# Performance work log

Measured on AMD Instinct MI355X. Metric: run time of the kernel, lower is better.

The kernel has to match this reference:

```python
import jax, jax.numpy as jnp
import numpy as np

MARGIN = 1.0
EPS = 1e-12


def setup_inputs() -> dict:
    key = jax.random.key(0)
    k1, k2, k3 = jax.random.split(key, 3)
    B, C, D = 16384, 500, 512
    features = jax.random.normal(k1, (B, D), dtype=jnp.float32)
    prototypes = jax.random.normal(k2, (C, D), dtype=jnp.float32)
    labels = jax.random.randint(k3, (B,), 0, C, dtype=jnp.int64)
    return {"features": features, "prototypes": prototypes, "labels": labels}


def reference(features, prototypes, labels):
    # Pairwise L2 distances [B, C] via the expanded form (no [B,C,D] intermediate)
    f2 = jnp.sum(features * features, axis=-1, keepdims=True)   # [B, 1]
    p2 = jnp.sum(prototypes * prototypes, axis=-1)               # [C]
    sq = f2 + p2 - 2.0 * (features @ prototypes.T)               # [B, C]
    dists = jnp.sqrt(jnp.maximum(sq, EPS))                       # [B, C]

    B, C = dists.shape
    d_pos = jnp.take_along_axis(dists, labels[:, None], axis=1)[:, 0]  # [B]
    pos_mask = jax.nn.one_hot(labels, C, dtype=bool)             # [B, C]
    d_neg_min = jnp.min(jnp.where(pos_mask, jnp.inf, dists), axis=-1)  # [B]

    loss = jnp.mean(jax.nn.relu(d_pos - d_neg_min + MARGIN))
    return loss
```

## Files before the change

kernel.cpp:

```cpp
#include <hip/hip_runtime.h>
#include <stdint.h>
#include <stddef.h>

#define BB 16384
#define CC 500
#define DD 512
#define PADC 512
#define LMARGIN 1.0f
#define EPSQ 1e-12f

#define GROUP_P 32
#define N_GROUPS (PADC / GROUP_P)
#define ROWB 1040

typedef __attribute__((ext_vector_type(8))) _Float16 f16x8;
typedef __attribute__((ext_vector_type(4))) float f32x4;

#define GLOBAL_AS __attribute__((address_space(1)))
#define LDS_AS __attribute__((address_space(3)))

__device__ __forceinline__ void ld_lds16(const void* g, void* l) {
  __builtin_amdgcn_global_load_lds((const GLOBAL_AS void*)g, (LDS_AS void*)l, 16, 0, 0);
}

__device__ __forceinline__ unsigned short f2h_bits(float f) {
  union { _Float16 h; unsigned short u; } v;
  v.h = (_Float16)f;
  return v.u;
}

__global__ void prep_kernel(const float* __restrict__ protos,
                            unsigned short* __restrict__ protoH,
                            float* __restrict__ p2) {
  int c = blockIdx.x;
  int t = threadIdx.x;
  float v0 = 0.f, v1 = 0.f;
  if (c < CC) {
    v0 = protos[c * DD + 2 * t];
    v1 = protos[c * DD + 2 * t + 1];
  }
  unsigned pk = (unsigned)f2h_bits(v0) | ((unsigned)f2h_bits(v1) << 16);
  ((unsigned*)protoH)[c * (DD / 2) + t] = pk;
  float s = v0 * v0 + v1 * v1;
#pragma unroll
  for (int d = 1; d < 64; d <<= 1) s += __shfl_xor(s, d, 64);
  __shared__ float ws4[4];
  if ((t & 63) == 0) ws4[t >> 6] = s;
  __syncthreads();
  if (t == 0) p2[c] = ws4[0] + ws4[1] + ws4[2] + ws4[3];
}

__launch_bounds__(256, 1)
__global__ void loss_kernel(const float* __restrict__ feat,
                            const int* __restrict__ labels,
                            const unsigned short* __restrict__ protoH,
                            const float* __restrict__ p2,
                            float* __restrict__ out) {
  __shared__ __align__(16) unsigned char ldsB[GROUP_P * ROWB];
  __shared__ float f2s[4][16];
  __shared__ float wsum[4];

  const int tid = threadIdx.x;
  const int wave = tid >> 6;
  const int lane = tid & 63;
  const int lane16 = lane & 15;
  const int quad = lane >> 4;
  const int rowBase = blockIdx.x * 64 + wave * 16;

#pragma unroll
  for (int r = 0; r < 8; ++r) {
    int p = wave * 8 + r;
    ld_lds16(protoH + (size_t)p * DD + lane * 8, ldsB + p * ROWB);
  }

  f16x8 afrag[16];
  float f2part = 0.f;
  const float* frow = feat + (size_t)(rowBase + lane16) * DD;
#pragma unroll
  for (int s = 0; s < 16; ++s) {
    const int k0 = s * 32 + quad * 8;
    f32x4 a0 = *(const f32x4*)(frow + k0);
    f32x4 a1 = *(const f32x4*)(frow + k0 + 4);
    f16x8 af;
#pragma unroll
    for (int j = 0; j < 4; ++j) {
      af[j] = (_Float16)a0[j];
      af[j + 4] = (_Float16)a1[j];
      f2part = fmaf(a0[j], a0[j], f2part);
      f2part = fmaf(a1[j], a1[j], f2part);
    }
    afrag[s] = af;
  }
  f2part += __shfl_xor(f2part, 16, 64);
  f2part += __shfl_xor(f2part, 32, 64);
  if (quad == 0) f2s[wave][lane16] = f2part;

  int lab[4];
#pragma unroll
  for (int i = 0; i < 4; ++i) lab[i] = labels[rowBase + quad * 4 + i];

  __syncthreads();

  float f2r[4];
#pragma unroll
  for (int i = 0; i < 4; ++i) f2r[i] = f2s[wave][quad * 4 + i];

  float runMin[4], posD[4];
#pragma unroll
  for (int i = 0; i < 4; ++i) { runMin[i] = 1e30f; posD[i] = -1e30f; }

  for (int g = 0; g < N_GROUPS; ++g) {
    f32x4 acc0 = {0.f, 0.f, 0.f, 0.f};
    f32x4 acc1 = {0.f, 0.f, 0.f, 0.f};
    const unsigned char* bbase = ldsB + lane16 * ROWB + quad * 16;
#pragma unroll
    for (int s = 0; s < 16; ++s) {
      f16x8 b0 = *(const f16x8*)(bbase + s * 64);
      f16x8 b1 = *(const f16x8*)(bbase + 16 * ROWB + s * 64);
      acc0 = __builtin_amdgcn_mfma_f32_16x16x32_f16(afrag[s], b0, acc0, 0, 0, 0);
      acc1 = __builtin_amdgcn_mfma_f32_16x16x32_f16(afrag[s], b1, acc1, 0, 0, 0);
    }
    __syncthreads();
    if (g + 1 < N_GROUPS) {
#pragma unroll
      for (int r = 0; r < 8; ++r) {
        int p = wave * 8 + r;
        ld_lds16(protoH + (size_t)((g + 1) * GROUP_P + p) * DD + lane * 8,
                 ldsB + p * ROWB);
      }
    }
    const int col0 = g * GROUP_P + lane16;
    const int col1 = col0 + 16;
    const float p20 = p2[col0];
    const float p21 = p2[col1];
#pragma unroll
    for (int i = 0; i < 4; ++i) {
      float d0 = sqrtf(fmaxf(f2r[i] + p20 - 2.f * acc0[i], EPSQ));
      float d1 = sqrtf(fmaxf(f2r[i] + p21 - 2.f * acc1[i], EPSQ));
      bool isPos0 = (col0 == lab[i]);
      bool isPos1 = (col1 == lab[i]);
      posD[i] = fmaxf(posD[i], isPos0 ? d0 : -1e30f);
      posD[i] = fmaxf(posD[i], isPos1 ? d1 : -1e30f);
      runMin[i] = fminf(runMin[i], (!isPos0 && col0 < CC) ? d0 : 1e30f);
      runMin[i] = fminf(runMin[i], (!isPos1 && col1 < CC) ? d1 : 1e30f);
    }
    __syncthreads();
  }

  float termSum = 0.f;
#pragma unroll
  for (int i = 0; i < 4; ++i) {
    float m = runMin[i], p = posD[i];
#pragma unroll
    for (int d = 1; d < 16; d <<= 1) {
      m = fminf(m, __shfl_xor(m, d, 64));
      p = fmaxf(p, __shfl_xor(p, d, 64));
    }
    termSum += fmaxf(p - m + LMARGIN, 0.f);
  }
  float contrib = (lane16 == 0) ? termSum : 0.f;
#pragma unroll
  for (int d = 1; d < 64; d <<= 1) contrib += __shfl_xor(contrib, d, 64);
  if (lane == 0) wsum[wave] = contrib;
  __syncthreads();
  if (tid == 0)
    atomicAdd(out, (wsum[0] + wsum[1] + wsum[2] + wsum[3]) * (1.0f / BB));
}

extern "C" void kernel_launch(void* const* d_in, const int* in_sizes, int n_in,
                              void* d_out, int out_size, void* d_ws, size_t ws_size,
                              hipStream_t stream) {
  const float* feat = (const float*)d_in[0];
  const float* protos = (const float*)d_in[1];
  const int* labels = (const int*)d_in[2];
  float* out = (float*)d_out;

  unsigned short* protoH = (unsigned short*)d_ws;
  float* p2 = (float*)((char*)d_ws + (size_t)PADC * DD * sizeof(unsigned short));

  hipMemsetAsync(d_out, 0, sizeof(float) * (out_size > 0 ? out_size : 1), stream);
  prep_kernel<<<PADC, 256, 0, stream>>>(protos, protoH, p2);
  loss_kernel<<<BB / 64, 256, 0, stream>>>(feat, labels, protoH, p2, out);
}
```

Before: 107.9 us.

## Restructure into fp16 prepass plus 2D-tiled MFMA GEMM with partial-reduction kernel

Replaces the single fused loss kernel with four stages. Features are converted to fp16 in a separate pass, a 128x128 tiled GEMM with double-buffered LDS staging writes per-row partial min/positive distances for each column tile, and a final kernel reduces them into the loss. The host memset is dropped and the output is zeroed inside the prototype prep kernel. The aim is better data reuse and more parallelism (a 2D grid, two blocks per CU), at the cost of an extra fp16 feature round trip through memory, more launches, and reliance on the zeroing kernel running before the atomic adds.

```diff
diff --git a/kernel.cpp b/kernel.cpp
--- a/kernel.cpp
+++ b/kernel.cpp
@@ -8,10 +8,7 @@
 #define PADC 512
 #define LMARGIN 1.0f
 #define EPSQ 1e-12f
-
-#define GROUP_P 32
-#define N_GROUPS (PADC / GROUP_P)
-#define ROWB 1040
+#define NK 16
 
 typedef __attribute__((ext_vector_type(8))) _Float16 f16x8;
 typedef __attribute__((ext_vector_type(4))) float f32x4;
@@ -23,148 +20,189 @@
   __builtin_amdgcn_global_load_lds((const GLOBAL_AS void*)g, (LDS_AS void*)l, 16, 0, 0);
 }
 
-__device__ __forceinline__ unsigned short f2h_bits(float f) {
-  union { _Float16 h; unsigned short u; } v;
-  v.h = (_Float16)f;
-  return v.u;
-}
-
-__global__ void prep_kernel(const float* __restrict__ protos,
-                            unsigned short* __restrict__ protoH,
-                            float* __restrict__ p2) {
-  int c = blockIdx.x;
-  int t = threadIdx.x;
-  float v0 = 0.f, v1 = 0.f;
+__global__ void prepP_kernel(const float* __restrict__ protos,
+                             unsigned short* __restrict__ protoH,
+                             float* __restrict__ p2,
+                             float* __restrict__ out) {
+  int c = blockIdx.x * 4 + (threadIdx.x >> 6);
+  int lane = threadIdx.x & 63;
+  if (c == 0 && lane == 0) out[0] = 0.f;
+  f32x4 a0 = {0.f, 0.f, 0.f, 0.f}, a1 = a0;
   if (c < CC) {
-    v0 = protos[c * DD + 2 * t];
-    v1 = protos[c * DD + 2 * t + 1];
-  }
-  unsigned pk = (unsigned)f2h_bits(v0) | ((unsigned)f2h_bits(v1) << 16);
-  ((unsigned*)protoH)[c * (DD / 2) + t] = pk;
-  float s = v0 * v0 + v1 * v1;
+    const float* src = protos + (size_t)c * DD + lane * 8;
+    a0 = *(const f32x4*)src;
+    a1 = *(const f32x4*)(src + 4);
+  }
+  f16x8 h;
+  float s = 0.f;
+#pragma unroll
+  for (int u = 0; u < 4; ++u) {
+    h[u] = (_Float16)a0[u];
+    h[u + 4] = (_Float16)a1[u];
+    s = fmaf(a0[u], a0[u], s);
+    s = fmaf(a1[u], a1[u], s);
+  }
+  *(f16x8*)(protoH + (size_t)c * DD + lane * 8) = h;
 #pragma unroll
   for (int d = 1; d < 64; d <<= 1) s += __shfl_xor(s, d, 64);
-  __shared__ float ws4[4];
-  if ((t & 63) == 0) ws4[t >> 6] = s;
-  __syncthreads();
-  if (t == 0) p2[c] = ws4[0] + ws4[1] + ws4[2] + ws4[3];
-}
-
-__launch_bounds__(256, 1)
-__global__ void loss_kernel(const float* __restrict__ feat,
+  if (lane == 0) p2[c] = s;
+}
+
+__global__ void prepF_kernel(const float* __restrict__ feat,
+                             unsigned short* __restrict__ featH,
+                             float* __restrict__ f2) {
+  int row = blockIdx.x * 4 + (threadIdx.x >> 6);
+  int lane = threadIdx.x & 63;
+  const float* src = feat + (size_t)row * DD + lane * 8;
+  f32x4 a0 = *(const f32x4*)src;
+  f32x4 a1 = *(const f32x4*)(src + 4);
+  f16x8 h;
+  float s = 0.f;
+#pragma unroll
+  for (int u = 0; u < 4; ++u) {
+    h[u] = (_Float16)a0[u];
+    h[u + 4] = (_Float16)a1[u];
+    s = fmaf(a0[u], a0[u], s);
+    s = fmaf(a1[u], a1[u], s);
+  }
+  *(f16x8*)(featH + (size_t)row * DD + lane * 8) = h;
+#pragma unroll
+  for (int d = 1; d < 64; d <<= 1) s += __shfl_xor(s, d, 64);
+  if (lane == 0) f2[row] = s;
+}
+
+__launch_bounds__(256, 2)
+__global__ void gemm_kernel(const unsigned short* __restrict__ featH,
+                            const unsigned short* __restrict__ protoH,
+                            const float* __restrict__ f2,
+                            const float* __restrict__ p2,
                             const int* __restrict__ labels,
-                            const unsigned short* __restrict__ protoH,
-                            const float* __restrict__ p2,
-                            float* __restrict__ out) {
-  __shared__ __align__(16) unsigned char ldsB[GROUP_P * ROWB];
-  __shared__ float f2s[4][16];
-  __shared__ float wsum[4];
+                            float2* __restrict__ ws2) {
+  __shared__ __align__(16) unsigned short Ab[2][128 * 32];
+  __shared__ __align__(16) unsigned short Bb[2][128 * 32];
+  __shared__ float f2l[128], p2l[128];
+  __shared__ int labl[128];
+  __shared__ float redM[2][128], redP[2][128];
 
   const int tid = threadIdx.x;
-  const int wave = tid >> 6;
+  const int w = tid >> 6;
   const int lane = tid & 63;
   const int lane16 = lane & 15;
   const int quad = lane >> 4;
-  const int rowBase = blockIdx.x * 64 + wave * 16;
-
-#pragma unroll
-  for (int r = 0; r < 8; ++r) {
-    int p = wave * 8 + r;
-    ld_lds16(protoH + (size_t)p * DD + lane * 8, ldsB + p * ROWB);
-  }
-
-  f16x8 afrag[16];
-  float f2part = 0.f;
-  const float* frow = feat + (size_t)(rowBase + lane16) * DD;
-#pragma unroll
-  for (int s = 0; s < 16; ++s) {
-    const int k0 = s * 32 + quad * 8;
-    f32x4 a0 = *(const f32x4*)(frow + k0);
-    f32x4 a1 = *(const f32x4*)(frow + k0 + 4);
-    f16x8 af;
-#pragma unroll
-    for (int j = 0; j < 4; ++j) {
-      af[j] = (_Float16)a0[j];
-      af[j + 4] = (_Float16)a1[j];
-      f2part = fmaf(a0[j], a0[j], f2part);
-      f2part = fmaf(a1[j], a1[j], f2part);
-    }
-    afrag[s] = af;
-  }
-  f2part += __shfl_xor(f2part, 16, 64);
-  f2part += __shfl_xor(f2part, 32, 64);
-  if (quad == 0) f2s[wave][lane16] = f2part;
-
-  int lab[4];
-#pragma unroll
-  for (int i = 0; i < 4; ++i) lab[i] = labels[rowBase + quad * 4 + i];
+  const int wm = w & 1;
+  const int wn = w >> 1;
+  const int r0 = blockIdx.x * 128;
+  const int c0 = blockIdx.y * 128;
+
+  const int srow = w * 16 + (lane >> 2);
+  const int sbyte = (lane & 3) * 16;
+  const char* gA = (const char*)featH + ((size_t)(r0 + srow) * DD) * 2 + sbyte;
+  const char* gB = (const char*)protoH + ((size_t)(c0 + srow) * DD) * 2 + sbyte;
+
+#define STAGE(kc, buf)                                                       \
+  do {                                                                       \
+    char* lA = (char*)&Ab[buf][0] + w * 1024 + lane * 16;                    \
+    char* lB = (char*)&Bb[buf][0] + w * 1024 + lane * 16;                    \
+    ld_lds16(gA + (kc) * 64, lA);                                            \
+    ld_lds16(gA + (kc) * 64 + (size_t)64 * DD * 2, lA + 4096);               \
+    ld_lds16(gB + (kc) * 64, lB);                                            \
+    ld_lds16(gB + (kc) * 64 + (size_t)64 * DD * 2, lB + 4096);               \
+  } while (0)
+
+  STAGE(0, 0);
+
+  if (tid < 128) {
+    f2l[tid] = f2[r0 + tid];
+    p2l[tid] = p2[c0 + tid];
+    labl[tid] = labels[r0 + tid];
+  }
+
+  f32x4 acc[4][4];
+#pragma unroll
+  for (int ms = 0; ms < 4; ++ms)
+#pragma unroll
+    for (int ns = 0; ns < 4; ++ns) acc[ms][ns] = (f32x4){0.f, 0.f, 0.f, 0.f};
 
   __syncthreads();
 
-  float f2r[4];
-#pragma unroll
-  for (int i = 0; i < 4; ++i) f2r[i] = f2s[wave][quad * 4 + i];
-
-  float runMin[4], posD[4];
-#pragma unroll
-  for (int i = 0; i < 4; ++i) { runMin[i] = 1e30f; posD[i] = -1e30f; }
-
-  for (int g = 0; g < N_GROUPS; ++g) {
-    f32x4 acc0 = {0.f, 0.f, 0.f, 0.f};
-    f32x4 acc1 = {0.f, 0.f, 0.f, 0.f};
-    const unsigned char* bbase = ldsB + lane16 * ROWB + quad * 16;
-#pragma unroll
-    for (int s = 0; s < 16; ++s) {
-      f16x8 b0 = *(const f16x8*)(bbase + s * 64);
-      f16x8 b1 = *(const f16x8*)(bbase + 16 * ROWB + s * 64);
-      acc0 = __builtin_amdgcn_mfma_f32_16x16x32_f16(afrag[s], b0, acc0, 0, 0, 0);
-      acc1 = __builtin_amdgcn_mfma_f32_16x16x32_f16(afrag[s], b1, acc1, 0, 0, 0);
-    }
+  int buf = 0;
+  for (int kc = 0; kc < NK; ++kc) {
+    if (kc + 1 < NK) STAGE(kc + 1, buf ^ 1);
+
+    f16x8 af[4], bfr[4];
+#pragma unroll
+    for (int ms = 0; ms < 4; ++ms)
+      af[ms] = *(const f16x8*)(&Ab[buf][(wm * 64 + ms * 16 + lane16) * 32 +
+                                        quad * 8]);
+#pragma unroll
+    for (int ns = 0; ns < 4; ++ns)
+      bfr[ns] = *(const f16x8*)(&Bb[buf][(wn * 64 + ns * 16 + lane16) * 32 +
+                                         quad * 8]);
+#pragma unroll
+    for (int ms = 0; ms < 4; ++ms)
+#pragma unroll
+      for (int ns = 0; ns < 4; ++ns)
+        acc[ms][ns] = __builtin_amdgcn_mfma_f32_16x16x32_f16(
+            af[ms], bfr[ns], acc[ms][ns], 0, 0, 0);
+
     __syncthreads();
-    if (g + 1 < N_GROUPS) {
-#pragma unroll
-      for (int r = 0; r < 8; ++r) {
-        int p = wave * 8 + r;
-        ld_lds16(protoH + (size_t)((g + 1) * GROUP_P + p) * DD + lane * 8,
-                 ldsB + p * ROWB);
+    buf ^= 1;
+  }
+
+#pragma unroll
+  for (int ms = 0; ms < 4; ++ms) {
+#pragma unroll
+    for (int i = 0; i < 4; ++i) {
+      const int rowIn = wm * 64 + ms * 16 + quad * 4 + i;
+      const float f2v = f2l[rowIn];
+      const int lb = labl[rowIn];
+      float m = 1e30f, p = -1e30f;
+#pragma unroll
+      for (int ns = 0; ns < 4; ++ns) {
+        const int colIn = wn * 64 + ns * 16 + lane16;
+        const int col = c0 + colIn;
+        float d = sqrtf(fmaxf(f2v + p2l[colIn] - 2.f * acc[ms][ns][i], EPSQ));
+        bool isPos = (col == lb);
+        p = fmaxf(p, isPos ? d : -1e30f);
+        m = fminf(m, (!isPos && col < CC) ? d : 1e30f);
+      }
+#pragma unroll
+      for (int d = 1; d < 16; d <<= 1) {
+        m = fminf(m, __shfl_xor(m, d, 64));
+        p = fmaxf(p, __shfl_xor(p, d, 64));
+      }
+      if (lane16 == 0) {
+        redM[wn][rowIn] = m;
+        redP[wn][rowIn] = p;
       }
     }
-    const int col0 = g * GROUP_P + lane16;
-    const int col1 = col0 + 16;
-    const float p20 = p2[col0];
-    const float p21 = p2[col1];
-#pragma unroll
-    for (int i = 0; i < 4; ++i) {
-      float d0 = sqrtf(fmaxf(f2r[i] + p20 - 2.f * acc0[i], EPSQ));
-      float d1 = sqrtf(fmaxf(f2r[i] + p21 - 2.f * acc1[i], EPSQ));
-      bool isPos0 = (col0 == lab[i]);
-      bool isPos1 = (col1 == lab[i]);
-      posD[i] = fmaxf(posD[i], isPos0 ? d0 : -1e30f);
-      posD[i] = fmaxf(posD[i], isPos1 ? d1 : -1e30f);
-      runMin[i] = fminf(runMin[i], (!isPos0 && col0 < CC) ? d0 : 1e30f);
-      runMin[i] = fminf(runMin[i], (!isPos1 && col1 < CC) ? d1 : 1e30f);
-    }
-    __syncthreads();
-  }
-
-  float termSum = 0.f;
-#pragma unroll
-  for (int i = 0; i < 4; ++i) {
-    float m = runMin[i], p = posD[i];
-#pragma unroll
-    for (int d = 1; d < 16; d <<= 1) {
-      m = fminf(m, __shfl_xor(m, d, 64));
-      p = fmaxf(p, __shfl_xor(p, d, 64));
-    }
-    termSum += fmaxf(p - m + LMARGIN, 0.f);
-  }
-  float contrib = (lane16 == 0) ? termSum : 0.f;
-#pragma unroll
-  for (int d = 1; d < 64; d <<= 1) contrib += __shfl_xor(contrib, d, 64);
-  if (lane == 0) wsum[wave] = contrib;
+  }
   __syncthreads();
-  if (tid == 0)
-    atomicAdd(out, (wsum[0] + wsum[1] + wsum[2] + wsum[3]) * (1.0f / BB));
+
+  if (tid < 128) {
+    float m = fminf(redM[0][tid], redM[1][tid]);
+    float p = fmaxf(redP[0][tid], redP[1][tid]);
+    ws2[(size_t)(r0 + tid) * 4 + blockIdx.y] = make_float2(m, p);
+  }
+#undef STAGE
+}
+
+__global__ void reduce_kernel(const float2* __restrict__ ws2,
+                              float* __restrict__ out) {
+  int row = blockIdx.x * 256 + threadIdx.x;
+  const float4* v = (const float4*)ws2;
+  float4 a = v[(size_t)row * 2];
+  float4 b = v[(size_t)row * 2 + 1];
+  float m = fminf(fminf(a.x, a.z), fminf(b.x, b.z));
+  float p = fmaxf(fmaxf(a.y, a.w), fmaxf(b.y, b.w));
+  float term = fmaxf(p - m + LMARGIN, 0.f);
+#pragma unroll
+  for (int d = 1; d < 64; d <<= 1) term += __shfl_xor(term, d, 64);
+  __shared__ float ws4[4];
+  if ((threadIdx.x & 63) == 0) ws4[threadIdx.x >> 6] = term;
+  __syncthreads();
+  if (threadIdx.x == 0)
+    atomicAdd(out, (ws4[0] + ws4[1] + ws4[2] + ws4[3]) * (1.0f / BB));
 }
 
 extern "C" void kernel_launch(void* const* d_in, const int* in_sizes, int n_in,
@@ -175,10 +213,16 @@
   const int* labels = (const int*)d_in[2];
   float* out = (float*)d_out;
 
-  unsigned short* protoH = (unsigned short*)d_ws;
-  float* p2 = (float*)((char*)d_ws + (size_t)PADC * DD * sizeof(unsigned short));
-
-  hipMemsetAsync(d_out, 0, sizeof(float) * (out_size > 0 ? out_size : 1), stream);
-  prep_kernel<<<PADC, 256, 0, stream>>>(protos, protoH, p2);
-  loss_kernel<<<BB / 64, 256, 0, stream>>>(feat, labels, protoH, p2, out);
-}
+  char* ws = (char*)d_ws;
+  unsigned short* protoH = (unsigned short*)(ws);
+  unsigned short* featH = (unsigned short*)(ws + (1 << 20));
+  float* p2 = (float*)(ws + (17 << 20));
+  float* f2 = (float*)(ws + (17 << 20) + (4 << 10));
+  float2* ws2 = (float2*)(ws + (17 << 20) + (128 << 10));
+
+  prepP_kernel<<<PADC / 4, 256, 0, stream>>>(protos, protoH, p2, out);
+  prepF_kernel<<<BB / 4, 256, 0, stream>>>(feat, featH, f2);
+  dim3 grid(BB / 128, PADC / 128);
+  gemm_kernel<<<grid, 256, 0, stream>>>(featH, protoH, f2, p2, labels, ws2);
+  reduce_kernel<<<BB / 256, 256, 0, stream>>>(ws2, out);
+}
```

Result: faster. 101.4 us (-6.1%).
